# Kernel optimization log

Measured on AMD Instinct MI355X. Metric: run time of the kernel, lower is better.

The kernel has to match this reference:

```python
import math
import jax, jax.numpy as jnp
import numpy as np

R = 4  # upsample_factor
C_FEAT = 22
FEAT_SLICES = {4: (0, 9), 6: (9, 22)}
SH_SLICES = {0: (0, 1), 2: (1, 6)}
AGG_PATHS = [(4, 0, 4), (4, 2, 4), (4, 2, 6), (6, 0, 6), (6, 2, 4), (6, 2, 6)]
TP_PATHS = [(4, 4, 4), (4, 4, 6), (4, 6, 4), (4, 6, 6), (6, 4, 4), (6, 4, 6), (6, 6, 4), (6, 6, 6)]
AGG_NPATH = {4: 3, 6: 3}
TP_NPATH = {4: 4, 6: 4}


def _cg(j1, m1, j2, m2, j3, m3):
    # Condon-Shortley Clebsch-Gordan <j1 m1 j2 m2 | j3 m3> (Racah formula)
    if m1 + m2 != m3:
        return 0.0
    f = math.factorial
    pre = (2 * j3 + 1) * f(j1 + j2 - j3) * f(j1 - j2 + j3) * f(-j1 + j2 + j3) / f(j1 + j2 + j3 + 1)
    pre *= f(j1 + m1) * f(j1 - m1) * f(j2 + m2) * f(j2 - m2) * f(j3 + m3) * f(j3 - m3)
    kmin = max(0, j2 - j3 - m1, j1 - j3 + m2)
    kmax = min(j1 + j2 - j3, j1 - m1, j2 + m2)
    s = 0.0
    for k in range(kmin, kmax + 1):
        s += (-1) ** k / (f(k) * f(j1 + j2 - j3 - k) * f(j1 - m1 - k) * f(j2 + m2 - k) * f(j3 - j2 + m1 + k) * f(j3 - j1 - m2 + k))
    return math.sqrt(pre) * s


def _q(l):
    # change of basis real SH -> complex SH (rows: real m, cols: complex m), with (-i)^l phase
    q = np.zeros((2 * l + 1, 2 * l + 1), dtype=np.complex128)
    q[l, l] = 1.0
    s2 = 1.0 / math.sqrt(2.0)
    for m in range(1, l + 1):
        q[l + m, l + m] = (-1) ** m * s2
        q[l + m, l - m] = s2
        q[l - m, l - m] = 1j * s2
        q[l - m, l + m] = -1j * (-1) ** m * s2
    return ((-1j) ** l) * q


def _w3j_real(l1, l2, l3):
    # Wigner 3j tensor in the real spherical-harmonic basis (invariant, unit Frobenius norm)
    w = np.zeros((2 * l1 + 1, 2 * l2 + 1, 2 * l3 + 1))
    for m1 in range(-l1, l1 + 1):
        for m2 in range(-l2, l2 + 1):
            m3 = -(m1 + m2)
            if abs(m3) <= l3:
                w[l1 + m1, l2 + m2, l3 + m3] = ((-1) ** (l1 - l2 - m3)) / math.sqrt(2 * l3 + 1) * _cg(l1, m1, l2, m2, l3, -m3)
    c = np.einsum('ai,bj,ck,ijk->abc', _q(l1), _q(l2), _q(l3), w.astype(np.complex128))
    return np.real(c).astype(np.float32)  # l1+l2+l3 even -> real


CG = {p: jnp.asarray(_w3j_real(*p)) for p in set(AGG_PATHS) | set(TP_PATHS)}


def _sh_kernel():
    # even-l real SH (integral normalization) at the 4 fixed 2x2 kernel directions
    s = 1.0 / math.sqrt(2.0)
    dirs = np.array([[-s, -s, 0.0], [s, -s, 0.0], [-s, s, 0.0], [s, s, 0.0]])
    x, y, z = dirs[:, 0], dirs[:, 1], dirs[:, 2]
    c2 = math.sqrt(15.0 / math.pi)
    sh = np.stack([
        np.full(4, 0.5 / math.sqrt(math.pi)),      # l=0
        0.5 * c2 * x * y,                           # l=2, m=-2
        0.5 * c2 * y * z,                           # l=2, m=-1
        0.25 * math.sqrt(5.0 / math.pi) * (3 * z ** 2 - 1.0),  # l=2, m=0
        0.5 * c2 * x * z,                           # l=2, m=1
        0.25 * c2 * (x ** 2 - y ** 2),              # l=2, m=2
    ], axis=1)
    return jnp.asarray(sh.astype(np.float32))  # (4, 6)


SH_KERNEL = _sh_kernel()


def setup_inputs() -> dict:
    key = jax.random.key(0)
    k1, k2, k3, k4 = jax.random.split(key, 4)
    H = W = 256
    return {
        'f4': jax.random.normal(k1, (H * W, 9), dtype=jnp.float32),
        'f6': jax.random.normal(k2, (H * W, 13), dtype=jnp.float32),
        'img_h': H,
        'img_w': W,
        'w_agg': jax.random.normal(k3, (6,), dtype=jnp.float32) * 0.1,
        'w_tp': jax.random.normal(k4, (8,), dtype=jnp.float32) * 0.1,
    }


def reference(f4, f6, img_h, img_w, w_agg, w_tp):
    H, W = int(img_h), int(img_w)
    Hr, Wr = H * R, W * R
    N = Hr * Wr
    # 1. nearest-neighbour upsample of concatenated irreps (H,W,22) -> (Hr,Wr,22)
    feat = jnp.concatenate([f4, f6], axis=-1).reshape(H, W, C_FEAT)
    feat_hr = jnp.repeat(jnp.repeat(feat, R, axis=0), R, axis=1)
    # 2. gather 2x2 patches with replicate padding (matches unfold k ordering (dh,dw))
    pad = jnp.pad(feat_hr, ((0, 1), (0, 1), (0, 0)), mode='edge')
    patches = jnp.stack([pad[dh:dh + Hr, dw:dw + Wr] for dh, dw in ((0, 0), (0, 1), (1, 0), (1, 1))], axis=2)
    patches = patches.reshape(N, 4, C_FEAT)  # (N,4,22)
    # tp_aggregate(neighbour, sh) summed over the 4 neighbours -> context (N,22)
    context = jnp.zeros((N, C_FEAT), dtype=feat.dtype)
    for i, (l1, l2, l3) in enumerate(AGG_PATHS):
        a0, a1 = FEAT_SLICES[l1]
        b0, b1 = SH_SLICES[l2]
        c0, c1 = FEAT_SLICES[l3]
        alpha = math.sqrt((2 * l3 + 1) / AGG_NPATH[l3])
        contrib = jnp.einsum('nka,kb,abc->nc', patches[:, :, a0:a1], SH_KERNEL[:, b0:b1], CG[(l1, l2, l3)])
        context = context.at[:, c0:c1].add((w_agg[i] * alpha) * contrib)
    # 3. tp(feat_self, context)
    feat_flat = feat_hr.reshape(N, C_FEAT)
    out = jnp.zeros((N, C_FEAT), dtype=feat.dtype)
    for i, (l1, l2, l3) in enumerate(TP_PATHS):
        a0, a1 = FEAT_SLICES[l1]
        b0, b1 = FEAT_SLICES[l2]
        c0, c1 = FEAT_SLICES[l3]
        alpha = math.sqrt((2 * l3 + 1) / TP_NPATH[l3])
        contrib = jnp.einsum('na,nb,abc->nc', feat_flat[:, a0:a1], context[:, b0:b1], CG[(l1, l2, l3)])
        out = out.at[:, c0:c1].add((w_tp[i] * alpha) * contrib)
    # 4. residual from the NN-upsampled features
    f4_out = out[:, :9] + feat_flat[:, :9]
    f6_out = out[:, 9:] + feat_flat[:, 9:]
    return f4_out, f6_out, (Hr, Wr)
```

## Files before the change

### kernel.cpp

```cpp
#include <hip/hip_runtime.h>
#include <hip/hip_bf16.h>
#include <math.h>

typedef __attribute__((ext_vector_type(8))) short short8;
typedef __attribute__((ext_vector_type(4))) float f32x4;
typedef __attribute__((ext_vector_type(2))) float f32x2;

__constant__ float c_fact[20] = {
    1.0f, 1.0f, 2.0f, 6.0f, 24.0f, 120.0f, 720.0f, 5040.0f, 40320.0f, 362880.0f,
    3628800.0f, 39916800.0f, 479001600.0f, 6227020800.0f, 87178291200.0f,
    1307674368000.0f, 20922789888000.0f, 355687428096000.0f,
    6402373705728000.0f, 121645100408832000.0f};
__constant__ float c_invf[20] = {
    1.0f, 1.0f, 0.5f, 0.16666666666666666f, 0.041666666666666664f,
    0.008333333333333333f, 0.001388888888888889f, 1.984126984126984e-4f,
    2.48015873015873e-5f, 2.755731922398589e-6f, 2.755731922398589e-7f,
    2.505210838544172e-8f, 2.08767569878681e-9f, 1.6059043836821613e-10f,
    1.1470745597729725e-11f, 7.647163731819816e-13f, 4.779477332387385e-14f,
    2.8114572543455206e-15f, 1.5619206968586225e-16f, 8.22063524662433e-18f};

__device__ float cgd(int j1, int m1, int j2, int m2, int j3, int m3) {
  if (m1 + m2 != m3) return 0.0f;
  float pre = (float)(2 * j3 + 1) * c_fact[j1 + j2 - j3] * c_fact[j1 - j2 + j3] *
              c_fact[-j1 + j2 + j3] * c_invf[j1 + j2 + j3 + 1];
  pre *= c_fact[j1 + m1] * c_fact[j1 - m1] * c_fact[j2 + m2] * c_fact[j2 - m2] *
         c_fact[j3 + m3] * c_fact[j3 - m3];
  int kmin = max(0, max(j2 - j3 - m1, j1 - j3 + m2));
  int kmax = min(j1 + j2 - j3, min(j1 - m1, j2 + m2));
  float s = 0.0f;
  for (int k = kmin; k <= kmax; ++k) {
    float d = c_invf[k] * c_invf[j1 + j2 - j3 - k] * c_invf[j1 - m1 - k] *
              c_invf[j2 + m2 - k] * c_invf[j3 - j2 + m1 + k] * c_invf[j3 - j1 - m2 + k];
    s += ((k & 1) ? -d : d);
  }
  return sqrtf(pre) * s;
}

__device__ float wstd(int l1, int l2, int l3, int i, int j, int k) {
  int m1 = i - l1, m2 = j - l2, m3 = k - l3;
  if (m1 + m2 + m3 != 0) return 0.0f;
  int e = l1 - l2 - m3;
  float sgn = (e & 1) ? -1.0f : 1.0f;
  return sgn * (1.0f / sqrtf((float)(2 * l3 + 1))) * cgd(l1, m1, l2, m2, l3, -m3);
}

__device__ int qrow(int l, int a, int idx[2], float vr[2], float vi[2]) {
  const float s2 = 0.70710678118654752440f;
  int m = a - l;
  if (m == 0) { idx[0] = l; vr[0] = 1.0f; vi[0] = 0.0f; return 1; }
  if (m > 0) {
    idx[0] = l + m; vr[0] = (m & 1) ? -s2 : s2; vi[0] = 0.0f;
    idx[1] = l - m; vr[1] = s2;                 vi[1] = 0.0f;
    return 2;
  }
  int mm = -m;
  idx[0] = l - mm; vr[0] = 0.0f; vi[0] = s2;
  idx[1] = l + mm; vr[1] = 0.0f; vi[1] = (mm & 1) ? s2 : -s2;
  return 2;
}

__device__ float w3j_real(int l1, int l2, int l3, int a, int b, int c) {
  int i1[2], i2[2], i3[2];
  float r1[2], s1[2], r2[2], s2v[2], r3[2], s3[2];
  int n1 = qrow(l1, a, i1, r1, s1);
  int n2 = qrow(l2, b, i2, r2, s2v);
  int n3 = qrow(l3, c, i3, r3, s3);
  float re = 0.0f;
  for (int x = 0; x < n1; ++x)
    for (int y = 0; y < n2; ++y)
      for (int z = 0; z < n3; ++z) {
        float w = wstd(l1, l2, l3, i1[x], i2[y], i3[z]);
        if (w == 0.0f) continue;
        float pr = r1[x] * r2[y] - s1[x] * s2v[y];
        float pi = r1[x] * s2v[y] + s1[x] * r2[y];
        float qr = pr * r3[z] - pi * s3[z];
        re += qr * w;
      }
  int L = l1 + l2 + l3;
  return ((L & 3) == 0) ? re : -re;
}

__device__ float sh_val(int k, int col) {
  const float PI_ = 3.14159265358979323846f;
  float sgn = (k == 0 || k == 3) ? 1.0f : -1.0f;
  if (col == 0) return 0.5f / sqrtf(PI_);
  if (col == 1) return sgn * 0.25f * sqrtf(15.0f / PI_);
  if (col == 3) return -0.25f * sqrtf(5.0f / PI_);
  return 0.0f;
}

__device__ __forceinline__ unsigned short bf16u(float x) {
  __hip_bfloat16 h = __float2bfloat16(x);
  return __builtin_bit_cast(unsigned short, h);
}
__device__ __forceinline__ float b2f(unsigned short u) {
  unsigned int v = ((unsigned int)u) << 16;
  return __builtin_bit_cast(float, v);
}

__global__ void eq_setup(const float* __restrict__ w_agg, const float* __restrict__ w_tp,
                         const int* __restrict__ ph, const int* __restrict__ pw,
                         float* __restrict__ out, long long tail_off,
                         unsigned short* __restrict__ ws) {
  int gid = blockIdx.x * 256 + threadIdx.x;
  if (gid == 0) {
    out[tail_off]     = (float)(ph[0] * 4);
    out[tail_off + 1] = (float)(pw[0] * 4);
  }
  if (gid < 22528) {
    int a = gid >> 10;
    int rem = gid & 1023;
    int nt = rem >> 9;
    int l = (rem >> 3) & 63;
    int e = rem & 7;
    int b = ((l >> 4) << 3) + e;
    int c = nt * 16 + (l & 15);
    float v = 0.f;
    if (b < 22 && c < 22) {
      int l1 = (a < 9) ? 4 : 6, l2 = (b < 9) ? 4 : 6, l3 = (c < 9) ? 4 : 6;
      int a_ = (a < 9) ? a : a - 9, b_ = (b < 9) ? b : b - 9, c_ = (c < 9) ? c : c - 9;
      int idx = ((l1 == 6) ? 4 : 0) + ((l2 == 6) ? 2 : 0) + ((l3 == 6) ? 1 : 0);
      float alpha = sqrtf((float)(2 * l3 + 1) * 0.25f);
      v = w_tp[idx] * alpha * w3j_real(l1, l2, l3, a_, b_, c_);
    }
    int pk = __builtin_amdgcn_cvt_pk_fp8_f32(v, 0.f, 0, 0);
    ((unsigned char*)ws)[gid] = (unsigned char)(pk & 0xff);
  } else if (gid < 26624) {
    int s = gid - 22528;
    int km = s >> 10;
    int rem = s & 1023;
    int nt = rem >> 9;
    int l = (rem >> 3) & 63;
    int e = rem & 7;
    int a = ((l >> 4) << 3) + e;
    int c = nt * 16 + (l & 15);
    float v = 0.f;
    if (a < 22 && c < 22) {
      int l1 = (a < 9) ? 4 : 6, l3 = (c < 9) ? 4 : 6;
      int a_ = (a < 9) ? a : a - 9, c_ = (c < 9) ? c : c - 9;
      float acc = 0.0f;
      float alpha = sqrtf((float)(2 * l3 + 1) / 3.0f);
      if (l1 == l3) {
        int i = (l1 == 4) ? 0 : 3;
        acc += w_agg[i] * alpha * sh_val(km, 0) * w3j_real(l1, 0, l3, a_, 0, c_);
      }
      {
        int i = (l1 == 4) ? ((l3 == 4) ? 1 : 2) : ((l3 == 4) ? 4 : 5);
        float t = 0.0f;
        for (int bb = 0; bb < 5; ++bb) {
          float shv = sh_val(km, 1 + bb);
          if (shv != 0.0f) t += shv * w3j_real(l1, 2, l3, a_, bb, c_);
        }
        acc += w_agg[i] * alpha * t;
      }
      v = acc;
    }
    ws[11264 + s] = bf16u(v);
  }
}

__device__ __forceinline__ void load_lds16(const unsigned int* g, unsigned int* l) {
  __builtin_amdgcn_global_load_lds(
      (const __attribute__((address_space(1))) unsigned int*)g,
      (__attribute__((address_space(3))) unsigned int*)l, 16, 0, 0);
}

#define WAVE_LDS_FENCE() do { \
    asm volatile("s_waitcnt lgkmcnt(0)" ::: "memory"); \
    __builtin_amdgcn_sched_barrier(0); } while (0)

__global__ __launch_bounds__(512, 8) void eq_main(
    const float* __restrict__ f4, const float* __restrict__ f6,
    const int* __restrict__ ph, const int* __restrict__ pw,
    const unsigned short* __restrict__ ws, float* __restrict__ out) {
  const int H = ph[0], Wc = pw[0];
  const int bx = (Wc + 31) >> 5;
  const long long ntiles = (long long)bx * H;

  __shared__ __align__(16) unsigned short LDS[15360];

  const int tid = threadIdx.x;
  const int wv = tid >> 6;
  const int l = tid & 63;
  const long long t = blockIdx.x;

  {
    const unsigned int* src = (const unsigned int*)ws;
    unsigned int* dst = (unsigned int*)LDS;
#pragma unroll
    for (int i = 0; i < 3; ++i) {
      int chunk = i * 8 + wv;
      if (chunk < 22) load_lds16(src + chunk * 256 + l * 4, dst + chunk * 256);
    }
  }

  short8 mb[8];
  {
    const short8* msrc = (const short8*)(ws + 11264);
#pragma unroll
    for (int i = 0; i < 8; ++i) mb[i] = msrc[i * 64 + l];
  }

  const int y0 = (int)(t / bx);
  const int xC0 = (int)(t - (long long)y0 * bx) << 5;
  const int cw0 = xC0 + (wv << 2);
  const int SOFF = 11264 + (wv << 9);
#pragma unroll
  for (int k = 0; k < 2; ++k) {
    int e = k * 64 + l;
    if (e < 110) {
      int px = e / 11, pr = e - px * 11;
      int dyR = px / 5, col = px - dyR * 5;
      int yy = min(y0 + dyR, H - 1);
      int xx = min(cw0 + col, Wc - 1);
      long long p = (long long)yy * Wc + xx;
      int ca = 2 * pr, cb = ca + 1;
      float v0 = (ca < 9) ? f4[p * 9 + ca] : f6[p * 13 + ca - 9];
      float v1 = (cb < 9) ? f4[p * 9 + cb] : f6[p * 13 + cb - 9];
      unsigned int pk = (unsigned int)bf16u(v0) | ((unsigned int)bf16u(v1) << 16);
      *(unsigned int*)&LDS[SOFF + px * 24 + ca] = pk;
    } else if (e < 120) {
      int px = e - 110;
      *(unsigned int*)&LDS[SOFF + px * 24 + 22] = 0u;
    }
  }

  __syncthreads();
  if (t >= ntiles) return;

  const int l15 = l & 15;
  const int lg = l >> 4;
  const int q = l15 & 3;
  const int lcell = l15 >> 2;
  const int a0 = lg << 3;

  f32x4 c0 = {0.f, 0.f, 0.f, 0.f}, c1 = {0.f, 0.f, 0.f, 0.f};
#pragma unroll
  for (int km = 0; km < 4; ++km) {
    short8 av = (short8)0;
    if (a0 < 24) {
      int dy = (km >> 1) & (q >> 1);
      int dx = km & q & 1;
      av = *(const short8*)&LDS[SOFF + (dy * 5 + lcell + dx) * 24 + a0];
    }
    c0 = __builtin_amdgcn_mfma_f32_16x16x32_bf16(av, mb[2 * km], c0, 0, 0, 0);
    c1 = __builtin_amdgcn_mfma_f32_16x16x32_bf16(av, mb[2 * km + 1], c1, 0, 0, 0);
  }

  unsigned int fvp[11];
  {
    const unsigned int* fp = (const unsigned int*)&LDS[SOFF + lcell * 24];
#pragma unroll
    for (int j = 0; j < 11; ++j) fvp[j] = fp[j];
  }
  const float r4 = b2f(LDS[SOFF + lg * 24 + l15]);
  const float r6 = (l15 < 6) ? b2f(LDS[SOFF + lg * 24 + 16 + l15]) : 0.f;
  WAVE_LDS_FENCE();

#pragma unroll
  for (int r = 0; r < 4; ++r) {
    LDS[SOFF + l15 * 24 + (lg << 2) + r] = bf16u(c0[r]);
    int ch1 = 16 + (lg << 2) + r;
    if (ch1 < 22) LDS[SOFF + l15 * 24 + ch1] = bf16u(c1[r]);
  }
  if (lg == 0) *(unsigned int*)&LDS[SOFF + l15 * 24 + 22] = 0u;
  WAVE_LDS_FENCE();

  f32x2 cv2[4];
  {
    short8 cvb = (short8)0;
    if (a0 < 24) cvb = *(const short8*)&LDS[SOFF + l15 * 24 + a0];
#pragma unroll
    for (int j = 0; j < 4; ++j) {
      cv2[j][0] = b2f((unsigned short)cvb[2 * j]);
      cv2[j][1] = b2f((unsigned short)cvb[2 * j + 1]);
    }
  }

  f32x4 oE0 = {0.f, 0.f, 0.f, 0.f}, oE1 = {0.f, 0.f, 0.f, 0.f};
  f32x4 oO0 = {0.f, 0.f, 0.f, 0.f}, oO1 = {0.f, 0.f, 0.f, 0.f};
  const char* Wb = (const char*)LDS;
#pragma unroll
  for (int ap = 0; ap < 11; ++ap) {
    const float sE = __builtin_bit_cast(float, fvp[ap] << 16);
    const float sO = __builtin_bit_cast(float, fvp[ap] & 0xffff0000u);
    {
      const f32x2 s2 = {sE, sE};
      f32x2 p0 = cv2[0] * s2, p1 = cv2[1] * s2, p2 = cv2[2] * s2, p3 = cv2[3] * s2;
      int lo = __builtin_amdgcn_cvt_pk_fp8_f32(p0[0], p0[1], 0, 0);
      lo = __builtin_amdgcn_cvt_pk_fp8_f32(p1[0], p1[1], lo, 1);
      int hi = __builtin_amdgcn_cvt_pk_fp8_f32(p2[0], p2[1], 0, 0);
      hi = __builtin_amdgcn_cvt_pk_fp8_f32(p3[0], p3[1], hi, 1);
      long av = (long)(((unsigned long long)(unsigned int)hi << 32) | (unsigned int)lo);
      long w0 = *(const long*)(Wb + ap * 2048 + l * 8);
      long w1 = *(const long*)(Wb + ap * 2048 + 512 + l * 8);
      oE0 = __builtin_amdgcn_mfma_f32_16x16x32_fp8_fp8(av, w0, oE0, 0, 0, 0);
      oE1 = __builtin_amdgcn_mfma_f32_16x16x32_fp8_fp8(av, w1, oE1, 0, 0, 0);
    }
    {
      const f32x2 s2 = {sO, sO};
      f32x2 p0 = cv2[0] * s2, p1 = cv2[1] * s2, p2 = cv2[2] * s2, p3 = cv2[3] * s2;
      int lo = __builtin_amdgcn_cvt_pk_fp8_f32(p0[0], p0[1], 0, 0);
      lo = __builtin_amdgcn_cvt_pk_fp8_f32(p1[0], p1[1], lo, 1);
      int hi = __builtin_amdgcn_cvt_pk_fp8_f32(p2[0], p2[1], 0, 0);
      hi = __builtin_amdgcn_cvt_pk_fp8_f32(p3[0], p3[1], hi, 1);
      long av = (long)(((unsigned long long)(unsigned int)hi << 32) | (unsigned int)lo);
      long w0 = *(const long*)(Wb + ap * 2048 + 1024 + l * 8);
      long w1 = *(const long*)(Wb + ap * 2048 + 1536 + l * 8);
      oO0 = __builtin_amdgcn_mfma_f32_16x16x32_fp8_fp8(av, w0, oO0, 0, 0, 0);
      oO1 = __builtin_amdgcn_mfma_f32_16x16x32_fp8_fp8(av, w1, oO1, 0, 0, 0);
    }
  }

#pragma unroll
  for (int r = 0; r < 4; ++r) {
    int n = (lg << 2) + r;
    LDS[SOFF + n * 24 + l15] = bf16u(oE0[r] + oO0[r] + r4);
    if (l15 < 6) LDS[SOFF + n * 24 + 16 + l15] = bf16u(oE1[r] + oO1[r] + r6);
  }
  WAVE_LDS_FENCE();

  {
    const int Wr = Wc << 2;
    const long long Npix = (long long)H * Wc * 16;
    float* out6 = out + Npix * 9;
    const int px = l & 15;
    const int ry = l >> 2 >> 2;
    const int n = (px & ~3) | ((ry == 3) ? 2 : 0) | (((px & 3) == 3) ? 1 : 0);
    const short8 r0 = *(const short8*)&LDS[SOFF + n * 24];
    const short8 r1 = *(const short8*)&LDS[SOFF + n * 24 + 8];
    const short8 r2 = *(const short8*)&LDS[SOFF + n * 24 + 16];
    const int hrx = (cw0 << 2) + px;
    if (hrx < Wr) {
      const long long rowb = (long long)((y0 << 2) + ry) * Wr + hrx;
      float* o4 = out + rowb * 9;
#pragma unroll
      for (int j = 0; j < 8; ++j) o4[j] = b2f((unsigned short)r0[j]);
      o4[8] = b2f((unsigned short)r1[0]);
      float* o6 = out6 + rowb * 13;
#pragma unroll
      for (int j = 0; j < 7; ++j) o6[j] = b2f((unsigned short)r1[1 + j]);
#pragma unroll
      for (int j = 0; j < 6; ++j) o6[7 + j] = b2f((unsigned short)r2[j]);
    }
  }
}

extern "C" void kernel_launch(void* const* d_in, const int* in_sizes, int n_in,
                              void* d_out, int out_size, void* d_ws, size_t ws_size,
                              hipStream_t stream) {
  const float* f4 = (const float*)d_in[0];
  const float* f6 = (const float*)d_in[1];
  const int* ph = (const int*)d_in[2];
  const int* pw = (const int*)d_in[3];
  const float* wagg = (const float*)d_in[4];
  const float* wtp = (const float*)d_in[5];
  float* out = (float*)d_out;
  unsigned short* wsu = (unsigned short*)d_ws;

  long long HW = (long long)in_sizes[0] / 9;
  long long tail = (long long)out_size - 2;

  eq_setup<<<104, 256, 0, stream>>>(wagg, wtp, ph, pw, out, tail, wsu);

  int S = (int)(sqrt((double)HW) + 0.5);
  long long nb;
  if ((long long)S * S == HW) {
    nb = (long long)((S + 31) / 32) * S;
  } else {
    nb = HW;
  }
  eq_main<<<(int)nb, 512, 0, stream>>>(f4, f6, ph, pw, wsu, out);
}
```

Measured before the change: 54.63 us.

## Process two tiles per block and prefetch second tile's inputs during first

Each block now handles two consecutive tiles. The MFMA B-fragments are moved into LDS alongside the weights, so the setup load is paid once per two tiles. The second tile's global feature loads are issued after the first tile's compute and before its output writes, to overlap load latency with the store phase. This halves the grid, grows LDS per block to 40KB, and may lower occupancy or raise register pressure from the prefetched values.

```diff
diff --git a/kernel.cpp b/kernel.cpp
--- a/kernel.cpp
+++ b/kernel.cpp
@@ -169,70 +169,12 @@
     asm volatile("s_waitcnt lgkmcnt(0)" ::: "memory"); \
     __builtin_amdgcn_sched_barrier(0); } while (0)
 
-__global__ __launch_bounds__(512, 8) void eq_main(
-    const float* __restrict__ f4, const float* __restrict__ f6,
-    const int* __restrict__ ph, const int* __restrict__ pw,
-    const unsigned short* __restrict__ ws, float* __restrict__ out) {
-  const int H = ph[0], Wc = pw[0];
-  const int bx = (Wc + 31) >> 5;
-  const long long ntiles = (long long)bx * H;
-
-  __shared__ __align__(16) unsigned short LDS[15360];
-
-  const int tid = threadIdx.x;
-  const int wv = tid >> 6;
-  const int l = tid & 63;
-  const long long t = blockIdx.x;
-
-  {
-    const unsigned int* src = (const unsigned int*)ws;
-    unsigned int* dst = (unsigned int*)LDS;
-#pragma unroll
-    for (int i = 0; i < 3; ++i) {
-      int chunk = i * 8 + wv;
-      if (chunk < 22) load_lds16(src + chunk * 256 + l * 4, dst + chunk * 256);
-    }
-  }
-
+__device__ __forceinline__ void compute_phase(
+    unsigned short* LDS, int SOFF, int COFF,
+    int l, int l15, int lg, int q, int lcell, int a0) {
   short8 mb[8];
-  {
-    const short8* msrc = (const short8*)(ws + 11264);
-#pragma unroll
-    for (int i = 0; i < 8; ++i) mb[i] = msrc[i * 64 + l];
-  }
-
-  const int y0 = (int)(t / bx);
-  const int xC0 = (int)(t - (long long)y0 * bx) << 5;
-  const int cw0 = xC0 + (wv << 2);
-  const int SOFF = 11264 + (wv << 9);
-#pragma unroll
-  for (int k = 0; k < 2; ++k) {
-    int e = k * 64 + l;
-    if (e < 110) {
-      int px = e / 11, pr = e - px * 11;
-      int dyR = px / 5, col = px - dyR * 5;
-      int yy = min(y0 + dyR, H - 1);
-      int xx = min(cw0 + col, Wc - 1);
-      long long p = (long long)yy * Wc + xx;
-      int ca = 2 * pr, cb = ca + 1;
-      float v0 = (ca < 9) ? f4[p * 9 + ca] : f6[p * 13 + ca - 9];
-      float v1 = (cb < 9) ? f4[p * 9 + cb] : f6[p * 13 + cb - 9];
-      unsigned int pk = (unsigned int)bf16u(v0) | ((unsigned int)bf16u(v1) << 16);
-      *(unsigned int*)&LDS[SOFF + px * 24 + ca] = pk;
-    } else if (e < 120) {
-      int px = e - 110;
-      *(unsigned int*)&LDS[SOFF + px * 24 + 22] = 0u;
-    }
-  }
-
-  __syncthreads();
-  if (t >= ntiles) return;
-
-  const int l15 = l & 15;
-  const int lg = l >> 4;
-  const int q = l15 & 3;
-  const int lcell = l15 >> 2;
-  const int a0 = lg << 3;
+#pragma unroll
+  for (int i = 0; i < 8; ++i) mb[i] = *(const short8*)&LDS[11264 + i * 512 + l * 8];
 
   f32x4 c0 = {0.f, 0.f, 0.f, 0.f}, c1 = {0.f, 0.f, 0.f, 0.f};
 #pragma unroll
@@ -259,17 +201,17 @@
 
 #pragma unroll
   for (int r = 0; r < 4; ++r) {
-    LDS[SOFF + l15 * 24 + (lg << 2) + r] = bf16u(c0[r]);
+    LDS[COFF + l15 * 24 + (lg << 2) + r] = bf16u(c0[r]);
     int ch1 = 16 + (lg << 2) + r;
-    if (ch1 < 22) LDS[SOFF + l15 * 24 + ch1] = bf16u(c1[r]);
-  }
-  if (lg == 0) *(unsigned int*)&LDS[SOFF + l15 * 24 + 22] = 0u;
+    if (ch1 < 22) LDS[COFF + l15 * 24 + ch1] = bf16u(c1[r]);
+  }
+  if (lg == 0) *(unsigned int*)&LDS[COFF + l15 * 24 + 22] = 0u;
   WAVE_LDS_FENCE();
 
   f32x2 cv2[4];
   {
     short8 cvb = (short8)0;
-    if (a0 < 24) cvb = *(const short8*)&LDS[SOFF + l15 * 24 + a0];
+    if (a0 < 24) cvb = *(const short8*)&LDS[COFF + l15 * 24 + a0];
 #pragma unroll
     for (int j = 0; j < 4; ++j) {
       cv2[j][0] = b2f((unsigned short)cvb[2 * j]);
@@ -315,34 +257,169 @@
 #pragma unroll
   for (int r = 0; r < 4; ++r) {
     int n = (lg << 2) + r;
-    LDS[SOFF + n * 24 + l15] = bf16u(oE0[r] + oO0[r] + r4);
-    if (l15 < 6) LDS[SOFF + n * 24 + 16 + l15] = bf16u(oE1[r] + oO1[r] + r6);
+    LDS[COFF + n * 24 + l15] = bf16u(oE0[r] + oO0[r] + r4);
+    if (l15 < 6) LDS[COFF + n * 24 + 16 + l15] = bf16u(oE1[r] + oO1[r] + r6);
   }
   WAVE_LDS_FENCE();
+}
+
+__device__ __forceinline__ void writer_phase(
+    const unsigned short* LDS, int COFF, int l,
+    int y0, int cw0, int Wr, float* out, float* out6) {
+  const int px = l & 15;
+  const int ry = l >> 4;
+  const int n = (px & ~3) | ((ry == 3) ? 2 : 0) | (((px & 3) == 3) ? 1 : 0);
+  const short8 r0 = *(const short8*)&LDS[COFF + n * 24];
+  const short8 r1 = *(const short8*)&LDS[COFF + n * 24 + 8];
+  const short8 r2 = *(const short8*)&LDS[COFF + n * 24 + 16];
+  const int hrx = (cw0 << 2) + px;
+  if (hrx < Wr) {
+    const long long rowb = (long long)((y0 << 2) + ry) * Wr + hrx;
+    float* o4 = out + rowb * 9;
+#pragma unroll
+    for (int j = 0; j < 8; ++j) o4[j] = b2f((unsigned short)r0[j]);
+    o4[8] = b2f((unsigned short)r1[0]);
+    float* o6 = out6 + rowb * 13;
+#pragma unroll
+    for (int j = 0; j < 7; ++j) o6[j] = b2f((unsigned short)r1[1 + j]);
+#pragma unroll
+    for (int j = 0; j < 6; ++j) o6[7 + j] = b2f((unsigned short)r2[j]);
+  }
+}
+
+__global__ __launch_bounds__(512, 8) void eq_main(
+    const float* __restrict__ f4, const float* __restrict__ f6,
+    const int* __restrict__ ph, const int* __restrict__ pw,
+    const unsigned short* __restrict__ ws, float* __restrict__ out) {
+  const int H = ph[0], Wc = pw[0];
+  const int bx = (Wc + 31) >> 5;
+  const long long ntiles = (long long)bx * H;
+  const int Wr = Wc << 2;
+  const long long Npix = (long long)H * Wc * 16;
+  float* out6 = out + Npix * 9;
+
+  __shared__ __align__(16) unsigned short LDS[20480];
+
+  const int tid = threadIdx.x;
+  const int wv = tid >> 6;
+  const int l = tid & 63;
+  const long long t0 = (long long)blockIdx.x * 2;
+  const long long t1 = t0 + 1;
+  const bool t0ok = t0 < ntiles;
+  const bool t1ok = t1 < ntiles;
 
   {
-    const int Wr = Wc << 2;
-    const long long Npix = (long long)H * Wc * 16;
-    float* out6 = out + Npix * 9;
-    const int px = l & 15;
-    const int ry = l >> 2 >> 2;
-    const int n = (px & ~3) | ((ry == 3) ? 2 : 0) | (((px & 3) == 3) ? 1 : 0);
-    const short8 r0 = *(const short8*)&LDS[SOFF + n * 24];
-    const short8 r1 = *(const short8*)&LDS[SOFF + n * 24 + 8];
-    const short8 r2 = *(const short8*)&LDS[SOFF + n * 24 + 16];
-    const int hrx = (cw0 << 2) + px;
-    if (hrx < Wr) {
-      const long long rowb = (long long)((y0 << 2) + ry) * Wr + hrx;
-      float* o4 = out + rowb * 9;
-#pragma unroll
-      for (int j = 0; j < 8; ++j) o4[j] = b2f((unsigned short)r0[j]);
-      o4[8] = b2f((unsigned short)r1[0]);
-      float* o6 = out6 + rowb * 13;
-#pragma unroll
-      for (int j = 0; j < 7; ++j) o6[j] = b2f((unsigned short)r1[1 + j]);
-#pragma unroll
-      for (int j = 0; j < 6; ++j) o6[7 + j] = b2f((unsigned short)r2[j]);
-    }
+    const unsigned int* src = (const unsigned int*)ws;
+    unsigned int* dst = (unsigned int*)LDS;
+#pragma unroll
+    for (int i = 0; i < 4; ++i) {
+      int chunk = i * 8 + wv;
+      if (chunk < 30) load_lds16(src + chunk * 256 + l * 4, dst + chunk * 256);
+    }
+  }
+
+  const int SOFF = 15360 + wv * 640;
+  const int COFF = SOFF + 256;
+
+  int y0 = 0, cw0 = 0;
+  if (t0ok) {
+    y0 = (int)(t0 / bx);
+    cw0 = ((int)(t0 - (long long)y0 * bx) << 5) + (wv << 2);
+#pragma unroll
+    for (int k = 0; k < 2; ++k) {
+      int e = k * 64 + l;
+      if (e < 110) {
+        int px = e / 11, pr = e - px * 11;
+        int dyR = px / 5, col = px - dyR * 5;
+        int yy = min(y0 + dyR, H - 1);
+        int xx = min(cw0 + col, Wc - 1);
+        long long p = (long long)yy * Wc + xx;
+        int ca = 2 * pr;
+        float v0 = (ca < 9) ? f4[p * 9 + ca] : f6[p * 13 + ca - 9];
+        float v1 = (ca + 1 < 9) ? f4[p * 9 + ca + 1] : f6[p * 13 + ca - 8];
+        unsigned int pk = (unsigned int)bf16u(v0) | ((unsigned int)bf16u(v1) << 16);
+        *(unsigned int*)&LDS[SOFF + px * 24 + ca] = pk;
+      } else if (e < 120) {
+        *(unsigned int*)&LDS[SOFF + (e - 110) * 24 + 22] = 0u;
+      }
+    }
+  }
+  __syncthreads();
+
+  const int l15 = l & 15;
+  const int lg = l >> 4;
+  const int q = l15 & 3;
+  const int lcell = l15 >> 2;
+  const int a0 = lg << 3;
+
+  int y1 = 0, cw1 = 0;
+  if (t1ok) {
+    y1 = (int)(t1 / bx);
+    cw1 = ((int)(t1 - (long long)y1 * bx) << 5) + (wv << 2);
+  }
+
+  if (t0ok) {
+    compute_phase(LDS, SOFF, COFF, l, l15, lg, q, lcell, a0);
+
+    float s_v0_0 = 0.f, s_v1_0 = 0.f, s_v0_1 = 0.f, s_v1_1 = 0.f;
+    if (t1ok) {
+      {
+        int e = l;
+        if (e < 110) {
+          int px = e / 11, pr = e - px * 11;
+          int dyR = px / 5, col = px - dyR * 5;
+          int yy = min(y1 + dyR, H - 1);
+          int xx = min(cw1 + col, Wc - 1);
+          long long p = (long long)yy * Wc + xx;
+          int ca = 2 * pr;
+          s_v0_0 = (ca < 9) ? f4[p * 9 + ca] : f6[p * 13 + ca - 9];
+          s_v1_0 = (ca + 1 < 9) ? f4[p * 9 + ca + 1] : f6[p * 13 + ca - 8];
+        }
+      }
+      {
+        int e = 64 + l;
+        if (e < 110) {
+          int px = e / 11, pr = e - px * 11;
+          int dyR = px / 5, col = px - dyR * 5;
+          int yy = min(y1 + dyR, H - 1);
+          int xx = min(cw1 + col, Wc - 1);
+          long long p = (long long)yy * Wc + xx;
+          int ca = 2 * pr;
+          s_v0_1 = (ca < 9) ? f4[p * 9 + ca] : f6[p * 13 + ca - 9];
+          s_v1_1 = (ca + 1 < 9) ? f4[p * 9 + ca + 1] : f6[p * 13 + ca - 8];
+        }
+      }
+      __builtin_amdgcn_sched_barrier(0);
+    }
+
+    writer_phase(LDS, COFF, l, y0, cw0, Wr, out, out6);
+
+    if (t1ok) {
+      {
+        int e = l;
+        if (e < 110) {
+          int px = e / 11, pr = e - px * 11;
+          unsigned int pk = (unsigned int)bf16u(s_v0_0) | ((unsigned int)bf16u(s_v1_0) << 16);
+          *(unsigned int*)&LDS[SOFF + px * 24 + 2 * pr] = pk;
+        } else if (e < 120) {
+          *(unsigned int*)&LDS[SOFF + (e - 110) * 24 + 22] = 0u;
+        }
+      }
+      {
+        int e = 64 + l;
+        if (e < 110) {
+          int px = e / 11, pr = e - px * 11;
+          unsigned int pk = (unsigned int)bf16u(s_v0_1) | ((unsigned int)bf16u(s_v1_1) << 16);
+          *(unsigned int*)&LDS[SOFF + px * 24 + 2 * pr] = pk;
+        }
+      }
+    }
+    WAVE_LDS_FENCE();
+  }
+
+  if (t1ok) {
+    compute_phase(LDS, SOFF, COFF, l, l15, lg, q, lcell, a0);
+    writer_phase(LDS, COFF, l, y1, cw1, Wr, out, out6);
   }
 }
 
@@ -366,9 +443,10 @@
   int S = (int)(sqrt((double)HW) + 0.5);
   long long nb;
   if ((long long)S * S == HW) {
-    nb = (long long)((S + 31) / 32) * S;
+    long long nt = (long long)((S + 31) / 32) * S;
+    nb = (nt + 1) / 2;
   } else {
-    nb = HW;
+    nb = HW / 2 + 2;
   }
   eq_main<<<(int)nb, 512, 0, stream>>>(f4, f6, ph, pw, wsu, out);
 }
```

Result: no change. 53.86 us (-1.4%).

## Keep TP weights in registers and process two cell groups per wave

Applied to the files above, without the earlier changes.

The fp8 tensor-product weight fragments now live in registers (44 longs per lane, loaded once from global) instead of being staged into shared memory with global_load_lds. Each wave now covers 8 coarse cells in two groups of 4, reusing the stencil halo and the loaded weights, so blocks are 256 threads with a much smaller shared-memory footprint. The block-wide __syncthreads is replaced by per-wave fences. The cost is much higher register pressure from the 44-entry weight array, which lowers occupancy (launch bounds 256,3) and could cause spilling.

```diff
diff --git a/kernel.cpp b/kernel.cpp
--- a/kernel.cpp
+++ b/kernel.cpp
@@ -159,74 +159,72 @@
   }
 }
 
-__device__ __forceinline__ void load_lds16(const unsigned int* g, unsigned int* l) {
-  __builtin_amdgcn_global_load_lds(
-      (const __attribute__((address_space(1))) unsigned int*)g,
-      (__attribute__((address_space(3))) unsigned int*)l, 16, 0, 0);
-}
-
 #define WAVE_LDS_FENCE() do { \
     asm volatile("s_waitcnt lgkmcnt(0)" ::: "memory"); \
     __builtin_amdgcn_sched_barrier(0); } while (0)
 
-__global__ __launch_bounds__(512, 8) void eq_main(
+__global__ __launch_bounds__(256, 3) void eq_main(
     const float* __restrict__ f4, const float* __restrict__ f6,
     const int* __restrict__ ph, const int* __restrict__ pw,
     const unsigned short* __restrict__ ws, float* __restrict__ out) {
   const int H = ph[0], Wc = pw[0];
   const int bx = (Wc + 31) >> 5;
   const long long ntiles = (long long)bx * H;
-
-  __shared__ __align__(16) unsigned short LDS[15360];
+  const int Wr = Wc << 2;
+  const long long Npix = (long long)H * Wc * 16;
+  float* out6 = out + Npix * 9;
+
+  __shared__ __align__(16) unsigned short LDS[4864];
 
   const int tid = threadIdx.x;
   const int wv = tid >> 6;
   const int l = tid & 63;
   const long long t = blockIdx.x;
-
-  {
-    const unsigned int* src = (const unsigned int*)ws;
-    unsigned int* dst = (unsigned int*)LDS;
-#pragma unroll
-    for (int i = 0; i < 3; ++i) {
-      int chunk = i * 8 + wv;
-      if (chunk < 22) load_lds16(src + chunk * 256 + l * 4, dst + chunk * 256);
-    }
-  }
+  if (t >= ntiles) return;
+
+  const int y0 = (int)(t / bx);
+  const int x0 = (int)(t - (long long)y0 * bx) << 5;
+  const int cwB = x0 + (wv << 3);
+  const int WOFF = wv * 1216;
 
   short8 mb[8];
   {
-    const short8* msrc = (const short8*)(ws + 11264);
-#pragma unroll
-    for (int i = 0; i < 8; ++i) mb[i] = msrc[i * 64 + l];
-  }
-
-  const int y0 = (int)(t / bx);
-  const int xC0 = (int)(t - (long long)y0 * bx) << 5;
-  const int cw0 = xC0 + (wv << 2);
-  const int SOFF = 11264 + (wv << 9);
-#pragma unroll
-  for (int k = 0; k < 2; ++k) {
-    int e = k * 64 + l;
-    if (e < 110) {
+    const unsigned short* msrc = ws + 11264;
+#pragma unroll
+    for (int i = 0; i < 8; ++i) mb[i] = *(const short8*)(msrc + i * 512 + l * 8);
+  }
+
+#pragma unroll
+  for (int it = 0; it < 4; ++it) {
+    int e = it * 64 + l;
+    if (e < 198) {
       int px = e / 11, pr = e - px * 11;
-      int dyR = px / 5, col = px - dyR * 5;
+      int dyR = px / 9, col = px - dyR * 9;
       int yy = min(y0 + dyR, H - 1);
-      int xx = min(cw0 + col, Wc - 1);
+      int xx = min(cwB + col, Wc - 1);
       long long p = (long long)yy * Wc + xx;
-      int ca = 2 * pr, cb = ca + 1;
+      int ca = 2 * pr;
       float v0 = (ca < 9) ? f4[p * 9 + ca] : f6[p * 13 + ca - 9];
-      float v1 = (cb < 9) ? f4[p * 9 + cb] : f6[p * 13 + cb - 9];
+      float v1 = (ca + 1 < 9) ? f4[p * 9 + ca + 1] : f6[p * 13 + ca - 8];
       unsigned int pk = (unsigned int)bf16u(v0) | ((unsigned int)bf16u(v1) << 16);
-      *(unsigned int*)&LDS[SOFF + px * 24 + ca] = pk;
-    } else if (e < 120) {
-      int px = e - 110;
-      *(unsigned int*)&LDS[SOFF + px * 24 + 22] = 0u;
-    }
-  }
-
-  __syncthreads();
-  if (t >= ntiles) return;
+      *(unsigned int*)&LDS[WOFF + px * 24 + ca] = pk;
+    } else if (e < 216) {
+      *(unsigned int*)&LDS[WOFF + (e - 198) * 24 + 22] = 0u;
+    }
+  }
+
+  long Wr_[44];
+  {
+    const char* wsb = (const char*)ws;
+#pragma unroll
+    for (int ap = 0; ap < 11; ++ap) {
+#pragma unroll
+      for (int j = 0; j < 4; ++j)
+        Wr_[ap * 4 + j] = *(const long*)(wsb + ap * 2048 + j * 512 + l * 8);
+    }
+  }
+
+  WAVE_LDS_FENCE();
 
   const int l15 = l & 15;
   const int lg = l >> 4;
@@ -234,114 +232,115 @@
   const int lcell = l15 >> 2;
   const int a0 = lg << 3;
 
-  f32x4 c0 = {0.f, 0.f, 0.f, 0.f}, c1 = {0.f, 0.f, 0.f, 0.f};
-#pragma unroll
-  for (int km = 0; km < 4; ++km) {
-    short8 av = (short8)0;
-    if (a0 < 24) {
-      int dy = (km >> 1) & (q >> 1);
-      int dx = km & q & 1;
-      av = *(const short8*)&LDS[SOFF + (dy * 5 + lcell + dx) * 24 + a0];
-    }
-    c0 = __builtin_amdgcn_mfma_f32_16x16x32_bf16(av, mb[2 * km], c0, 0, 0, 0);
-    c1 = __builtin_amdgcn_mfma_f32_16x16x32_bf16(av, mb[2 * km + 1], c1, 0, 0, 0);
-  }
-
-  unsigned int fvp[11];
-  {
-    const unsigned int* fp = (const unsigned int*)&LDS[SOFF + lcell * 24];
-#pragma unroll
-    for (int j = 0; j < 11; ++j) fvp[j] = fp[j];
-  }
-  const float r4 = b2f(LDS[SOFF + lg * 24 + l15]);
-  const float r6 = (l15 < 6) ? b2f(LDS[SOFF + lg * 24 + 16 + l15]) : 0.f;
+#pragma unroll
+  for (int g = 0; g < 2; ++g) {
+    const int COFF = WOFF + 448 + g * 384;
+    f32x4 c0 = {0.f, 0.f, 0.f, 0.f}, c1 = {0.f, 0.f, 0.f, 0.f};
+#pragma unroll
+    for (int km = 0; km < 4; ++km) {
+      short8 av = (short8)0;
+      if (a0 < 24) {
+        int dy = (km >> 1) & (q >> 1);
+        int dx = km & q & 1;
+        av = *(const short8*)&LDS[WOFF + (dy * 9 + (g << 2) + lcell + dx) * 24 + a0];
+      }
+      c0 = __builtin_amdgcn_mfma_f32_16x16x32_bf16(av, mb[2 * km], c0, 0, 0, 0);
+      c1 = __builtin_amdgcn_mfma_f32_16x16x32_bf16(av, mb[2 * km + 1], c1, 0, 0, 0);
+    }
+#pragma unroll
+    for (int r = 0; r < 4; ++r) {
+      LDS[COFF + l15 * 24 + (lg << 2) + r] = bf16u(c0[r]);
+      int ch1 = 16 + (lg << 2) + r;
+      if (ch1 < 22) LDS[COFF + l15 * 24 + ch1] = bf16u(c1[r]);
+    }
+    if (lg == 0) *(unsigned int*)&LDS[COFF + l15 * 24 + 22] = 0u;
+  }
   WAVE_LDS_FENCE();
 
 #pragma unroll
-  for (int r = 0; r < 4; ++r) {
-    LDS[SOFF + l15 * 24 + (lg << 2) + r] = bf16u(c0[r]);
-    int ch1 = 16 + (lg << 2) + r;
-    if (ch1 < 22) LDS[SOFF + l15 * 24 + ch1] = bf16u(c1[r]);
-  }
-  if (lg == 0) *(unsigned int*)&LDS[SOFF + l15 * 24 + 22] = 0u;
-  WAVE_LDS_FENCE();
-
-  f32x2 cv2[4];
-  {
-    short8 cvb = (short8)0;
-    if (a0 < 24) cvb = *(const short8*)&LDS[SOFF + l15 * 24 + a0];
-#pragma unroll
-    for (int j = 0; j < 4; ++j) {
-      cv2[j][0] = b2f((unsigned short)cvb[2 * j]);
-      cv2[j][1] = b2f((unsigned short)cvb[2 * j + 1]);
-    }
-  }
-
-  f32x4 oE0 = {0.f, 0.f, 0.f, 0.f}, oE1 = {0.f, 0.f, 0.f, 0.f};
-  f32x4 oO0 = {0.f, 0.f, 0.f, 0.f}, oO1 = {0.f, 0.f, 0.f, 0.f};
-  const char* Wb = (const char*)LDS;
-#pragma unroll
-  for (int ap = 0; ap < 11; ++ap) {
-    const float sE = __builtin_bit_cast(float, fvp[ap] << 16);
-    const float sO = __builtin_bit_cast(float, fvp[ap] & 0xffff0000u);
+  for (int g = 0; g < 2; ++g) {
+    const int COFF = WOFF + 448 + g * 384;
+    const int frow = WOFF + ((g << 2) + lcell) * 24;
+
+    f32x2 cv2[4];
     {
-      const f32x2 s2 = {sE, sE};
-      f32x2 p0 = cv2[0] * s2, p1 = cv2[1] * s2, p2 = cv2[2] * s2, p3 = cv2[3] * s2;
-      int lo = __builtin_amdgcn_cvt_pk_fp8_f32(p0[0], p0[1], 0, 0);
-      lo = __builtin_amdgcn_cvt_pk_fp8_f32(p1[0], p1[1], lo, 1);
-      int hi = __builtin_amdgcn_cvt_pk_fp8_f32(p2[0], p2[1], 0, 0);
-      hi = __builtin_amdgcn_cvt_pk_fp8_f32(p3[0], p3[1], hi, 1);
-      long av = (long)(((unsigned long long)(unsigned int)hi << 32) | (unsigned int)lo);
-      long w0 = *(const long*)(Wb + ap * 2048 + l * 8);
-      long w1 = *(const long*)(Wb + ap * 2048 + 512 + l * 8);
-      oE0 = __builtin_amdgcn_mfma_f32_16x16x32_fp8_fp8(av, w0, oE0, 0, 0, 0);
-      oE1 = __builtin_amdgcn_mfma_f32_16x16x32_fp8_fp8(av, w1, oE1, 0, 0, 0);
-    }
+      short8 cvb = (short8)0;
+      if (a0 < 24) cvb = *(const short8*)&LDS[COFF + l15 * 24 + a0];
+#pragma unroll
+      for (int j = 0; j < 4; ++j) {
+        cv2[j][0] = b2f((unsigned short)cvb[2 * j]);
+        cv2[j][1] = b2f((unsigned short)cvb[2 * j + 1]);
+      }
+    }
+    unsigned int fvp[11];
     {
-      const f32x2 s2 = {sO, sO};
-      f32x2 p0 = cv2[0] * s2, p1 = cv2[1] * s2, p2 = cv2[2] * s2, p3 = cv2[3] * s2;
-      int lo = __builtin_amdgcn_cvt_pk_fp8_f32(p0[0], p0[1], 0, 0);
-      lo = __builtin_amdgcn_cvt_pk_fp8_f32(p1[0], p1[1], lo, 1);
-      int hi = __builtin_amdgcn_cvt_pk_fp8_f32(p2[0], p2[1], 0, 0);
-      hi = __builtin_amdgcn_cvt_pk_fp8_f32(p3[0], p3[1], hi, 1);
-      long av = (long)(((unsigned long long)(unsigned int)hi << 32) | (unsigned int)lo);
-      long w0 = *(const long*)(Wb + ap * 2048 + 1024 + l * 8);
-      long w1 = *(const long*)(Wb + ap * 2048 + 1536 + l * 8);
-      oO0 = __builtin_amdgcn_mfma_f32_16x16x32_fp8_fp8(av, w0, oO0, 0, 0, 0);
-      oO1 = __builtin_amdgcn_mfma_f32_16x16x32_fp8_fp8(av, w1, oO1, 0, 0, 0);
-    }
-  }
-
-#pragma unroll
-  for (int r = 0; r < 4; ++r) {
-    int n = (lg << 2) + r;
-    LDS[SOFF + n * 24 + l15] = bf16u(oE0[r] + oO0[r] + r4);
-    if (l15 < 6) LDS[SOFF + n * 24 + 16 + l15] = bf16u(oE1[r] + oO1[r] + r6);
-  }
-  WAVE_LDS_FENCE();
-
-  {
-    const int Wr = Wc << 2;
-    const long long Npix = (long long)H * Wc * 16;
-    float* out6 = out + Npix * 9;
-    const int px = l & 15;
-    const int ry = l >> 2 >> 2;
-    const int n = (px & ~3) | ((ry == 3) ? 2 : 0) | (((px & 3) == 3) ? 1 : 0);
-    const short8 r0 = *(const short8*)&LDS[SOFF + n * 24];
-    const short8 r1 = *(const short8*)&LDS[SOFF + n * 24 + 8];
-    const short8 r2 = *(const short8*)&LDS[SOFF + n * 24 + 16];
-    const int hrx = (cw0 << 2) + px;
-    if (hrx < Wr) {
-      const long long rowb = (long long)((y0 << 2) + ry) * Wr + hrx;
-      float* o4 = out + rowb * 9;
-#pragma unroll
-      for (int j = 0; j < 8; ++j) o4[j] = b2f((unsigned short)r0[j]);
-      o4[8] = b2f((unsigned short)r1[0]);
-      float* o6 = out6 + rowb * 13;
-#pragma unroll
-      for (int j = 0; j < 7; ++j) o6[j] = b2f((unsigned short)r1[1 + j]);
-#pragma unroll
-      for (int j = 0; j < 6; ++j) o6[7 + j] = b2f((unsigned short)r2[j]);
+      const unsigned int* fp = (const unsigned int*)&LDS[frow];
+#pragma unroll
+      for (int j = 0; j < 11; ++j) fvp[j] = fp[j];
+    }
+    const float r4 = b2f(LDS[WOFF + ((g << 2) + lg) * 24 + l15]);
+    const float r6 = (l15 < 6) ? b2f(LDS[WOFF + ((g << 2) + lg) * 24 + 16 + l15]) : 0.f;
+
+    f32x4 oE0 = {0.f, 0.f, 0.f, 0.f}, oE1 = {0.f, 0.f, 0.f, 0.f};
+    f32x4 oO0 = {0.f, 0.f, 0.f, 0.f}, oO1 = {0.f, 0.f, 0.f, 0.f};
+#pragma unroll
+    for (int ap = 0; ap < 11; ++ap) {
+      const float sE = __builtin_bit_cast(float, fvp[ap] << 16);
+      const float sO = __builtin_bit_cast(float, fvp[ap] & 0xffff0000u);
+      {
+        const f32x2 s2 = {sE, sE};
+        f32x2 p0 = cv2[0] * s2, p1 = cv2[1] * s2, p2 = cv2[2] * s2, p3 = cv2[3] * s2;
+        int lo = __builtin_amdgcn_cvt_pk_fp8_f32(p0[0], p0[1], 0, 0);
+        lo = __builtin_amdgcn_cvt_pk_fp8_f32(p1[0], p1[1], lo, 1);
+        int hi = __builtin_amdgcn_cvt_pk_fp8_f32(p2[0], p2[1], 0, 0);
+        hi = __builtin_amdgcn_cvt_pk_fp8_f32(p3[0], p3[1], hi, 1);
+        long av = (long)(((unsigned long long)(unsigned int)hi << 32) | (unsigned int)lo);
+        oE0 = __builtin_amdgcn_mfma_f32_16x16x32_fp8_fp8(av, Wr_[ap * 4 + 0], oE0, 0, 0, 0);
+        oE1 = __builtin_amdgcn_mfma_f32_16x16x32_fp8_fp8(av, Wr_[ap * 4 + 1], oE1, 0, 0, 0);
+      }
+      {
+        const f32x2 s2 = {sO, sO};
+        f32x2 p0 = cv2[0] * s2, p1 = cv2[1] * s2, p2 = cv2[2] * s2, p3 = cv2[3] * s2;
+        int lo = __builtin_amdgcn_cvt_pk_fp8_f32(p0[0], p0[1], 0, 0);
+        lo = __builtin_amdgcn_cvt_pk_fp8_f32(p1[0], p1[1], lo, 1);
+        int hi = __builtin_amdgcn_cvt_pk_fp8_f32(p2[0], p2[1], 0, 0);
+        hi = __builtin_amdgcn_cvt_pk_fp8_f32(p3[0], p3[1], hi, 1);
+        long av = (long)(((unsigned long long)(unsigned int)hi << 32) | (unsigned int)lo);
+        oO0 = __builtin_amdgcn_mfma_f32_16x16x32_fp8_fp8(av, Wr_[ap * 4 + 2], oO0, 0, 0, 0);
+        oO1 = __builtin_amdgcn_mfma_f32_16x16x32_fp8_fp8(av, Wr_[ap * 4 + 3], oO1, 0, 0, 0);
+      }
+    }
+
+#pragma unroll
+    for (int r = 0; r < 4; ++r) {
+      int n = (lg << 2) + r;
+      LDS[COFF + n * 24 + l15] = bf16u(oE0[r] + oO0[r] + r4);
+      if (l15 < 6) LDS[COFF + n * 24 + 16 + l15] = bf16u(oE1[r] + oO1[r] + r6);
+    }
+    WAVE_LDS_FENCE();
+
+    {
+      const int cwg = cwB + (g << 2);
+      const int px = l & 15;
+      const int ry = l >> 4;
+      const int n = (px & ~3) | ((ry == 3) ? 2 : 0) | (((px & 3) == 3) ? 1 : 0);
+      const short8 r0 = *(const short8*)&LDS[COFF + n * 24];
+      const short8 r1 = *(const short8*)&LDS[COFF + n * 24 + 8];
+      const short8 r2 = *(const short8*)&LDS[COFF + n * 24 + 16];
+      const int hrx = (cwg << 2) + px;
+      if (hrx < Wr) {
+        const long long rowb = (long long)((y0 << 2) + ry) * Wr + hrx;
+        float* o4 = out + rowb * 9;
+#pragma unroll
+        for (int j = 0; j < 8; ++j) o4[j] = b2f((unsigned short)r0[j]);
+        o4[8] = b2f((unsigned short)r1[0]);
+        float* o6 = out6 + rowb * 13;
+#pragma unroll
+        for (int j = 0; j < 7; ++j) o6[j] = b2f((unsigned short)r1[1 + j]);
+#pragma unroll
+        for (int j = 0; j < 6; ++j) o6[7 + j] = b2f((unsigned short)r2[j]);
+      }
+      WAVE_LDS_FENCE();
     }
   }
 }
@@ -370,5 +369,5 @@
   } else {
     nb = HW;
   }
-  eq_main<<<(int)nb, 512, 0, stream>>>(f4, f6, ph, pw, wsu, out);
-}
+  eq_main<<<(int)nb, 256, 0, stream>>>(f4, f6, ph, pw, wsu, out);
+}
```

Measured after the change: 58.55 us. 7.2% more time.

## Stage fp32 outputs in LDS as pixel-major rows for coalesced vector stores

Applied to the files above, without the earlier changes.

The epilogue now writes the per-cell results as fp32 into LDS, laid out as contiguous HR-pixel channel rows for the two distinct quadrant rows. Each wave then emits 16-byte vector stores covering whole contiguous output rows, replacing the per-lane scattered scalar stores. The context tensor is also kept in fp32 in LDS instead of bf16, and the early return moves before the LDS load. The larger LDS footprint and the lower launch_bounds occupancy hint (6 instead of 8) may reduce occupancy, and a fallback scalar path remains for edge tiles.

```diff
diff --git a/kernel.cpp b/kernel.cpp
--- a/kernel.cpp
+++ b/kernel.cpp
@@ -169,20 +169,29 @@
     asm volatile("s_waitcnt lgkmcnt(0)" ::: "memory"); \
     __builtin_amdgcn_sched_barrier(0); } while (0)
 
-__global__ __launch_bounds__(512, 8) void eq_main(
+__global__ __launch_bounds__(512, 6) void eq_main(
     const float* __restrict__ f4, const float* __restrict__ f6,
     const int* __restrict__ ph, const int* __restrict__ pw,
     const unsigned short* __restrict__ ws, float* __restrict__ out) {
   const int H = ph[0], Wc = pw[0];
   const int bx = (Wc + 31) >> 5;
   const long long ntiles = (long long)bx * H;
-
-  __shared__ __align__(16) unsigned short LDS[15360];
+  const int Wr = Wc << 2;
+  const long long Npix = (long long)H * Wc * 16;
+  float* out6 = out + Npix * 9;
+
+  __shared__ __align__(16) unsigned short LDS[23040];
 
   const int tid = threadIdx.x;
   const int wv = tid >> 6;
   const int l = tid & 63;
   const long long t = blockIdx.x;
+  if (t >= ntiles) return;
+
+  const int y0 = (int)(t / bx);
+  const int x0 = (int)(t - (long long)y0 * bx) << 5;
+  const int cw0 = x0 + (wv << 2);
+  const int SLOT = 11264 + wv * 1472;
 
   {
     const unsigned int* src = (const unsigned int*)ws;
@@ -196,15 +205,11 @@
 
   short8 mb[8];
   {
-    const short8* msrc = (const short8*)(ws + 11264);
-#pragma unroll
-    for (int i = 0; i < 8; ++i) mb[i] = msrc[i * 64 + l];
-  }
-
-  const int y0 = (int)(t / bx);
-  const int xC0 = (int)(t - (long long)y0 * bx) << 5;
-  const int cw0 = xC0 + (wv << 2);
-  const int SOFF = 11264 + (wv << 9);
+    const unsigned short* msrc = ws + 11264;
+#pragma unroll
+    for (int i = 0; i < 8; ++i) mb[i] = *(const short8*)(msrc + i * 512 + l * 8);
+  }
+
 #pragma unroll
   for (int k = 0; k < 2; ++k) {
     int e = k * 64 + l;
@@ -214,19 +219,17 @@
       int yy = min(y0 + dyR, H - 1);
       int xx = min(cw0 + col, Wc - 1);
       long long p = (long long)yy * Wc + xx;
-      int ca = 2 * pr, cb = ca + 1;
+      int ca = 2 * pr;
       float v0 = (ca < 9) ? f4[p * 9 + ca] : f6[p * 13 + ca - 9];
-      float v1 = (cb < 9) ? f4[p * 9 + cb] : f6[p * 13 + cb - 9];
+      float v1 = (ca + 1 < 9) ? f4[p * 9 + ca + 1] : f6[p * 13 + ca - 8];
       unsigned int pk = (unsigned int)bf16u(v0) | ((unsigned int)bf16u(v1) << 16);
-      *(unsigned int*)&LDS[SOFF + px * 24 + ca] = pk;
+      *(unsigned int*)&LDS[SLOT + px * 24 + ca] = pk;
     } else if (e < 120) {
-      int px = e - 110;
-      *(unsigned int*)&LDS[SOFF + px * 24 + 22] = 0u;
+      *(unsigned int*)&LDS[SLOT + (e - 110) * 24 + 22] = 0u;
     }
   }
 
   __syncthreads();
-  if (t >= ntiles) return;
 
   const int l15 = l & 15;
   const int lg = l >> 4;
@@ -241,7 +244,7 @@
     if (a0 < 24) {
       int dy = (km >> 1) & (q >> 1);
       int dx = km & q & 1;
-      av = *(const short8*)&LDS[SOFF + (dy * 5 + lcell + dx) * 24 + a0];
+      av = *(const short8*)&LDS[SLOT + (dy * 5 + lcell + dx) * 24 + a0];
     }
     c0 = __builtin_amdgcn_mfma_f32_16x16x32_bf16(av, mb[2 * km], c0, 0, 0, 0);
     c1 = __builtin_amdgcn_mfma_f32_16x16x32_bf16(av, mb[2 * km + 1], c1, 0, 0, 0);
@@ -249,33 +252,36 @@
 
   unsigned int fvp[11];
   {
-    const unsigned int* fp = (const unsigned int*)&LDS[SOFF + lcell * 24];
+    const unsigned int* fp = (const unsigned int*)&LDS[SLOT + lcell * 24];
 #pragma unroll
     for (int j = 0; j < 11; ++j) fvp[j] = fp[j];
   }
-  const float r4 = b2f(LDS[SOFF + lg * 24 + l15]);
-  const float r6 = (l15 < 6) ? b2f(LDS[SOFF + lg * 24 + 16 + l15]) : 0.f;
-  WAVE_LDS_FENCE();
-
+  const float r4 = b2f(LDS[SLOT + lg * 24 + l15]);
+  const float r6 = (l15 < 6) ? b2f(LDS[SLOT + lg * 24 + 16 + l15]) : 0.f;
+
+  float* ctxf = (float*)&LDS[SLOT + 256];
 #pragma unroll
   for (int r = 0; r < 4; ++r) {
-    LDS[SOFF + l15 * 24 + (lg << 2) + r] = bf16u(c0[r]);
+    ctxf[l15 * 24 + (lg << 2) + r] = c0[r];
     int ch1 = 16 + (lg << 2) + r;
-    if (ch1 < 22) LDS[SOFF + l15 * 24 + ch1] = bf16u(c1[r]);
-  }
-  if (lg == 0) *(unsigned int*)&LDS[SOFF + l15 * 24 + 22] = 0u;
+    if (ch1 < 22) ctxf[l15 * 24 + ch1] = c1[r];
+  }
+  if (lg == 0) { ctxf[l15 * 24 + 22] = 0.f; ctxf[l15 * 24 + 23] = 0.f; }
   WAVE_LDS_FENCE();
 
   f32x2 cv2[4];
   {
-    short8 cvb = (short8)0;
-    if (a0 < 24) cvb = *(const short8*)&LDS[SOFF + l15 * 24 + a0];
-#pragma unroll
-    for (int j = 0; j < 4; ++j) {
-      cv2[j][0] = b2f((unsigned short)cvb[2 * j]);
-      cv2[j][1] = b2f((unsigned short)cvb[2 * j + 1]);
-    }
-  }
+    f32x4 lo = {0.f, 0.f, 0.f, 0.f}, hi = {0.f, 0.f, 0.f, 0.f};
+    if (a0 < 24) {
+      lo = *(const f32x4*)(ctxf + l15 * 24 + a0);
+      hi = *(const f32x4*)(ctxf + l15 * 24 + a0 + 4);
+    }
+    cv2[0][0] = lo[0]; cv2[0][1] = lo[1];
+    cv2[1][0] = lo[2]; cv2[1][1] = lo[3];
+    cv2[2][0] = hi[0]; cv2[2][1] = hi[1];
+    cv2[3][0] = hi[2]; cv2[3][1] = hi[3];
+  }
+  WAVE_LDS_FENCE();
 
   f32x4 oE0 = {0.f, 0.f, 0.f, 0.f}, oE1 = {0.f, 0.f, 0.f, 0.f};
   f32x4 oO0 = {0.f, 0.f, 0.f, 0.f}, oO1 = {0.f, 0.f, 0.f, 0.f};
@@ -312,36 +318,53 @@
     }
   }
 
+  float* px4 = (float*)&LDS[SLOT];
+  float* px6 = px4 + 288;
 #pragma unroll
   for (int r = 0; r < 4; ++r) {
-    int n = (lg << 2) + r;
-    LDS[SOFF + n * 24 + l15] = bf16u(oE0[r] + oO0[r] + r4);
-    if (l15 < 6) LDS[SOFF + n * 24 + 16 + l15] = bf16u(oE1[r] + oO1[r] + r6);
+    const float v  = oE0[r] + oO0[r] + r4;
+    const float v1 = oE1[r] + oO1[r] + r6;
+    const int qy = r >> 1;
+    float* p4 = px4 + qy * 144;
+    float* p6 = px6 + qy * 208;
+    if (r & 1) {
+      const int px = (lg << 2) + 3;
+      if (l15 < 9) p4[px * 9 + l15] = v; else p6[px * 13 + l15 - 9] = v;
+      if (l15 < 6) p6[px * 13 + 7 + l15] = v1;
+    } else {
+#pragma unroll
+      for (int dx = 0; dx < 3; ++dx) {
+        const int px = (lg << 2) + dx;
+        if (l15 < 9) p4[px * 9 + l15] = v; else p6[px * 13 + l15 - 9] = v;
+        if (l15 < 6) p6[px * 13 + 7 + l15] = v1;
+      }
+    }
   }
   WAVE_LDS_FENCE();
 
-  {
-    const int Wr = Wc << 2;
-    const long long Npix = (long long)H * Wc * 16;
-    float* out6 = out + Npix * 9;
+  const long long y4 = (long long)(y0 << 2);
+  if (cw0 + 4 <= Wc) {
+#pragma unroll
+    for (int ry = 0; ry < 4; ++ry) {
+      const int qy = (ry == 3) ? 1 : 0;
+      float* o4p = out + ((y4 + ry) * Wr + (cw0 << 2)) * 9;
+      float* o6p = out6 + ((y4 + ry) * Wr + (cw0 << 2)) * 13;
+      if (l < 36) *(f32x4*)(o4p + (l << 2)) = *(const f32x4*)(px4 + qy * 144 + (l << 2));
+      if (l < 52) *(f32x4*)(o6p + (l << 2)) = *(const f32x4*)(px6 + qy * 208 + (l << 2));
+    }
+  } else {
     const int px = l & 15;
-    const int ry = l >> 2 >> 2;
-    const int n = (px & ~3) | ((ry == 3) ? 2 : 0) | (((px & 3) == 3) ? 1 : 0);
-    const short8 r0 = *(const short8*)&LDS[SOFF + n * 24];
-    const short8 r1 = *(const short8*)&LDS[SOFF + n * 24 + 8];
-    const short8 r2 = *(const short8*)&LDS[SOFF + n * 24 + 16];
+    const int ry = l >> 4;
+    const int qy = (ry == 3) ? 1 : 0;
     const int hrx = (cw0 << 2) + px;
     if (hrx < Wr) {
-      const long long rowb = (long long)((y0 << 2) + ry) * Wr + hrx;
+      const long long rowb = (y4 + ry) * Wr + hrx;
       float* o4 = out + rowb * 9;
-#pragma unroll
-      for (int j = 0; j < 8; ++j) o4[j] = b2f((unsigned short)r0[j]);
-      o4[8] = b2f((unsigned short)r1[0]);
       float* o6 = out6 + rowb * 13;
 #pragma unroll
-      for (int j = 0; j < 7; ++j) o6[j] = b2f((unsigned short)r1[1 + j]);
-#pragma unroll
-      for (int j = 0; j < 6; ++j) o6[7 + j] = b2f((unsigned short)r2[j]);
+      for (int ch = 0; ch < 9; ++ch) o4[ch] = px4[qy * 144 + px * 9 + ch];
+#pragma unroll
+      for (int ch = 0; ch < 13; ++ch) o6[ch] = px6[qy * 208 + px * 13 + ch];
     }
   }
 }
```

Result: faster. 46.09 us (median of 3 runs) (-15.6%).
